# Kernel optimization log

Measured on AMD Instinct MI355X. Metric: run time of the kernel, lower is better.

## Reference

```python
import jax, jax.numpy as jnp
import numpy as np

D, H, DH, L, DFF, V, K = 512, 8, 64, 6, 2048, 256, 5
N = 10240
TAU = 0.1
EPS = 1e-5


def _ln(x, w, b):
    m = x.mean(-1, keepdims=True)
    v = ((x - m) ** 2).mean(-1, keepdims=True)
    return (x - m) * jax.lax.rsqrt(v + EPS) * w + b


def _attn(q_in, kv_in, inw, inb, ow, ob):
    # q_in: [Q, D], kv_in: [M, D]; standard PyTorch MultiheadAttention math
    wq, wk, wv = jnp.split(inw, 3, 0)
    bq, bk, bv = jnp.split(inb, 3)
    q = (q_in @ wq.T + bq).reshape(-1, H, DH)
    k = (kv_in @ wk.T + bk).reshape(-1, H, DH)
    v = (kv_in @ wv.T + bv).reshape(-1, H, DH)
    s = jnp.einsum('qhd,mhd->hqm', q, k) / np.float32(np.sqrt(DH))
    o = jnp.einsum('hqm,mhd->qhd', jax.nn.softmax(s, -1), v).reshape(-1, D)
    return o @ ow.T + ob


def setup_inputs() -> dict:
    key = jax.random.key(0)
    ks = iter(jax.random.split(key, 64))

    def w(shape):
        return jax.random.normal(next(ks), shape, jnp.float32) * 0.02

    inp = {
        'input_bytes': jax.random.randint(next(ks), (N,), 0, V, jnp.int32),
        'emb': w((V, D)),
        'alpha': jnp.float32(0.5),
        'enc_inw': w((L, 3 * D, D)), 'enc_inb': w((L, 3 * D)),
        'enc_ow': w((L, D, D)), 'enc_ob': w((L, D)),
        'enc_w1': w((L, DFF, D)), 'enc_b1': w((L, DFF)),
        'enc_w2': w((L, D, DFF)), 'enc_b2': w((L, D)),
        'enc_ln1w': jnp.ones((L, D)), 'enc_ln1b': jnp.zeros((L, D)),
        'enc_ln2w': jnp.ones((L, D)), 'enc_ln2b': jnp.zeros((L, D)),
        'dec_sa_inw': w((L, 3 * D, D)), 'dec_sa_inb': w((L, 3 * D)),
        'dec_sa_ow': w((L, D, D)), 'dec_sa_ob': w((L, D)),
        'dec_ca_inw': w((L, 3 * D, D)), 'dec_ca_inb': w((L, 3 * D)),
        'dec_ca_ow': w((L, D, D)), 'dec_ca_ob': w((L, D)),
        'dec_w1': w((L, DFF, D)), 'dec_b1': w((L, DFF)),
        'dec_w2': w((L, D, DFF)), 'dec_b2': w((L, D)),
        'dec_ln1w': jnp.ones((L, D)), 'dec_ln1b': jnp.zeros((L, D)),
        'dec_ln2w': jnp.ones((L, D)), 'dec_ln2b': jnp.zeros((L, D)),
        'dec_ln3w': jnp.ones((L, D)), 'dec_ln3b': jnp.zeros((L, D)),
        'out_w': w((V, D)), 'out_b': w((V,)),
    }
    return inp


def reference(input_bytes, emb, alpha, enc_inw, enc_inb, enc_ow, enc_ob,
              enc_w1, enc_b1, enc_w2, enc_b2, enc_ln1w, enc_ln1b, enc_ln2w, enc_ln2b,
              dec_sa_inw, dec_sa_inb, dec_sa_ow, dec_sa_ob,
              dec_ca_inw, dec_ca_inb, dec_ca_ow, dec_ca_ob,
              dec_w1, dec_b1, dec_w2, dec_b2,
              dec_ln1w, dec_ln1b, dec_ln2w, dec_ln2b, dec_ln3w, dec_ln3b,
              out_w, out_b):
    P = input_bytes.shape[0] // K
    patches = input_bytes[:P * K].reshape(P, K)            # fixed k-byte patching
    x = emb[patches].mean(1)                               # mean-pooled patch embeddings [P, D]
    # ---- TransformerEncoder (post-LN, relu FFN, no dropout at eval) ----
    for l in range(L):
        x = _ln(x + _attn(x, x, enc_inw[l], enc_inb[l], enc_ow[l], enc_ob[l]), enc_ln1w[l], enc_ln1b[l])
        ff = jax.nn.relu(x @ enc_w1[l].T + enc_b1[l]) @ enc_w2[l].T + enc_b2[l]
        x = _ln(x + ff, enc_ln2w[l], enc_ln2b[l])
    encoded = x                                            # [P, D]
    # ---- gating + embedding mix (vectorized over the per-patch loop) ----
    gate = jnp.linalg.norm(encoded, axis=-1) > TAU
    tok = emb[patches[:, -1]]
    x = jnp.where(gate[:, None], alpha * encoded + (1.0 - alpha) * tok, tok)  # [P, D]
    # ---- TransformerDecoder: each patch is an independent length-1 target;
    #      self-attn over a single token reduces to out_proj(V(x));
    #      cross-attn attends to the full encoded memory (as in the original loop) ----
    for l in range(L):
        wv = dec_sa_inw[l][2 * D:]
        bv = dec_sa_inb[l][2 * D:]
        sa = (x @ wv.T + bv) @ dec_sa_ow[l].T + dec_sa_ob[l]
        x = _ln(x + sa, dec_ln1w[l], dec_ln1b[l])
        ca = _attn(x, encoded, dec_ca_inw[l], dec_ca_inb[l], dec_ca_ow[l], dec_ca_ob[l])
        x = _ln(x + ca, dec_ln2w[l], dec_ln2b[l])
        ff = jax.nn.relu(x @ dec_w1[l].T + dec_b1[l]) @ dec_w2[l].T + dec_b2[l]
        x = _ln(x + ff, dec_ln3w[l], dec_ln3b[l])
    return x @ out_w.T + out_b                             # [P, V]
```

## Files before the change

### kernel.cpp

```cpp
#include <hip/hip_runtime.h>
#include <hip/hip_bf16.h>
#include <math.h>

#define DD   512
#define HN   8
#define DHD  64
#define LL   6
#define DFF_ 2048
#define VV   256
#define KB_  5
#define PP   2048
#define EPS_ 1e-5f
#define TAU_ 0.1f
#define NS   4
#define KVS  (PP / NS)

typedef __attribute__((ext_vector_type(8))) short bf16x8;
typedef __attribute__((ext_vector_type(4))) short bf16x4;
typedef __attribute__((ext_vector_type(4))) float f32x4;

__device__ __forceinline__ float wave_sum(float v) {
#pragma unroll
  for (int m = 32; m >= 1; m >>= 1) v += __shfl_xor(v, m, 64);
  return v;
}

__device__ __forceinline__ unsigned short f2bf(float f) {
  unsigned u = __float_as_uint(f);
  u += 0x7FFF + ((u >> 16) & 1);
  return (unsigned short)(u >> 16);
}

__device__ __forceinline__ float bf2f(unsigned short u) {
  return __uint_as_float(((unsigned)u) << 16);
}

__device__ __forceinline__ bf16x8 cvt8(float4 a, float4 b) {
  bf16x8 v;
  v[0] = (short)f2bf(a.x); v[1] = (short)f2bf(a.y);
  v[2] = (short)f2bf(a.z); v[3] = (short)f2bf(a.w);
  v[4] = (short)f2bf(b.x); v[5] = (short)f2bf(b.y);
  v[6] = (short)f2bf(b.z); v[7] = (short)f2bf(b.w);
  return v;
}

__device__ __forceinline__ void gload16(const void* g, void* l) {
  __builtin_amdgcn_global_load_lds(
      (const __attribute__((address_space(1))) unsigned int*)g,
      (__attribute__((address_space(3))) unsigned int*)l, 16, 0, 0);
}

#define NSEG 55
struct CvtSeg { const float* src; short* dst; int n; };
struct CvtArgs { CvtSeg seg[NSEG]; };

__global__ __launch_bounds__(256) void convert_bf16_kernel(CvtArgs a) {
  const CvtSeg sg = a.seg[blockIdx.y];
  const int i = ((int)blockIdx.x * 256 + (int)threadIdx.x) * 16;
  if (i >= sg.n) return;
  const float4 x0 = *(const float4*)(sg.src + i);
  const float4 x1 = *(const float4*)(sg.src + i + 4);
  const float4 x2 = *(const float4*)(sg.src + i + 8);
  const float4 x3 = *(const float4*)(sg.src + i + 12);
  *(bf16x8*)(sg.dst + i)     = cvt8(x0, x1);
  *(bf16x8*)(sg.dst + i + 8) = cvt8(x2, x3);
}

__global__ __launch_bounds__(256) void transpose_wv_kernel(const float* __restrict__ sa_inw,
                                                           short* __restrict__ wvt) {
  __shared__ float t[64][65];
  const int l = blockIdx.z;
  const float* S = sa_inw + (size_t)l * 3 * DD * DD + (size_t)2 * DD * DD;
  short* D = wvt + (size_t)l * DD * DD;
  const int bo = blockIdx.y * 64;
  const int bi = blockIdx.x * 64;
  const int r = (int)threadIdx.x >> 2;
  const int c0 = ((int)threadIdx.x & 3) * 16;
#pragma unroll
  for (int j = 0; j < 16; j += 4)
    *(float4*)&t[r][c0 + j] = *(const float4*)&S[(size_t)(bo + r) * DD + bi + c0 + j];
  __syncthreads();
  bf16x8 o0, o1;
#pragma unroll
  for (int j = 0; j < 8; ++j) o0[j] = (short)f2bf(t[c0 + j][r]);
#pragma unroll
  for (int j = 0; j < 8; ++j) o1[j] = (short)f2bf(t[c0 + 8 + j][r]);
  short* dp = &D[(size_t)(bi + r) * DD + bo + c0];
  *(bf16x8*)dp = o0;
  *(bf16x8*)(dp + 8) = o1;
}

__global__ __launch_bounds__(256) void sa_bias_kernel(const float* __restrict__ sa_inb,
                                                      const float* __restrict__ sa_ow,
                                                      const float* __restrict__ sa_ob,
                                                      float* __restrict__ bc) {
  const int gid = (int)blockIdx.x * 4 + ((int)threadIdx.x >> 6);
  const int l = gid >> 9, n = gid & 511;
  const int lane = (int)threadIdx.x & 63;
  const float* wo = sa_ow + (size_t)l * DD * DD + (size_t)n * DD + lane * 8;
  const float* bv = sa_inb + (size_t)l * 3 * DD + 2 * DD + lane * 8;
  float s = 0.f;
#pragma unroll
  for (int j = 0; j < 8; ++j) s += wo[j] * bv[j];
  s = wave_sum(s);
  if (lane == 0) bc[(size_t)l * DD + n] = s + sa_ob[(size_t)l * DD + n];
}

__global__ __launch_bounds__(256) void gemm_wc_kernel(const short* __restrict__ WoBase,
                                                      size_t astr,
                                                      const short* __restrict__ WvT,
                                                      short* __restrict__ Wc) {
  constexpr int BK = 64;
  __shared__ short As[64 * BK];
  __shared__ short Bs[64 * BK];
  const int l = blockIdx.z;
  const short* A = WoBase + (size_t)l * astr;
  const short* W = WvT + (size_t)l * DD * DD;
  short* C = Wc + (size_t)l * DD * DD;
  const int tid = (int)threadIdx.x;
  const int lane = tid & 63;
  const int wid = tid >> 6;
  const int wm = (wid >> 1) * 32;
  const int wn = (wid & 1) * 32;
  const int bm = blockIdx.y * 64;
  const int bn = blockIdx.x * 64;
  const int fr = lane & 15;
  const int kq = lane >> 4;
  const int rs = fr & 7;
  const int srow = lane >> 3;
  const int scg = (lane & 7) ^ srow;

  f32x4 acc[2][2];
#pragma unroll
  for (int i = 0; i < 2; ++i)
#pragma unroll
    for (int j = 0; j < 2; ++j) acc[i][j] = (f32x4){0.f, 0.f, 0.f, 0.f};

  for (int k0 = 0; k0 < DD; k0 += BK) {
    __syncthreads();
#pragma unroll
    for (int is = 0; is < 2; ++is) {
      const int ib = is * 4 + wid;
      gload16(&A[(size_t)(bm + ib * 8 + srow) * DD + k0 + scg * 8], &As[ib * 512]);
      gload16(&W[(size_t)(bn + ib * 8 + srow) * DD + k0 + scg * 8], &Bs[ib * 512]);
    }
    __syncthreads();
#pragma unroll
    for (int s = 0; s < 2; ++s) {
      const int cg = s * 4 + kq;
      const int co = (cg ^ rs) * 8;
      bf16x8 af[2], bf[2];
#pragma unroll
      for (int i = 0; i < 2; ++i) af[i] = *(const bf16x8*)&As[(wm + i * 16 + fr) * BK + co];
#pragma unroll
      for (int j = 0; j < 2; ++j) bf[j] = *(const bf16x8*)&Bs[(wn + j * 16 + fr) * BK + co];
#pragma unroll
      for (int i = 0; i < 2; ++i)
#pragma unroll
        for (int j = 0; j < 2; ++j)
          acc[i][j] = __builtin_amdgcn_mfma_f32_16x16x32_bf16(af[i], bf[j], acc[i][j], 0, 0, 0);
    }
  }
  const int cr = (lane >> 4) * 4;
#pragma unroll
  for (int j = 0; j < 2; ++j) {
    const int col = bn + wn + j * 16 + fr;
#pragma unroll
    for (int i = 0; i < 2; ++i)
#pragma unroll
      for (int r = 0; r < 4; ++r)
        C[(size_t)(bm + wm + i * 16 + cr + r) * DD + col] = (short)f2bf(acc[i][j][r]);
  }
}

__global__ __launch_bounds__(256) void embed_mean_kernel(const int* __restrict__ bytes,
                                                         const float* __restrict__ emb,
                                                         float* __restrict__ x,
                                                         short* __restrict__ xb,
                                                         float* __restrict__ tok) {
  const int p = blockIdx.x;
  const int d = threadIdx.x * 2;
  float a0 = 0.f, a1 = 0.f;
  int last = 0;
#pragma unroll
  for (int k = 0; k < KB_; ++k) {
    const int idx = bytes[p * KB_ + k];
    last = idx;
    const float* e = emb + (size_t)idx * DD + d;
    a0 += e[0]; a1 += e[1];
  }
  a0 *= 0.2f; a1 *= 0.2f;
  x[(size_t)p * DD + d]     = a0;
  x[(size_t)p * DD + d + 1] = a1;
  xb[(size_t)p * DD + d]     = (short)f2bf(a0);
  xb[(size_t)p * DD + d + 1] = (short)f2bf(a1);
  const float* e = emb + (size_t)last * DD + d;
  tok[(size_t)p * DD + d]     = e[0];
  tok[(size_t)p * DD + d + 1] = e[1];
}

template <int BM, int BN, int NSPLIT, int RELU, int WF32, int WBF16, int QS>
__global__ __launch_bounds__(256) void gemm_gl_kernel(
    const short* __restrict__ A, int lda,
    const short* __restrict__ W, int ldw,
    const float* __restrict__ bias,
    float* __restrict__ Cf, short* __restrict__ Cb, int ldc, int Kd,
    size_t pstride) {
  constexpr int BK = 64;
  __shared__ short As[BM * BK];
  __shared__ short Bs[BN * BK];
  constexpr int WM = BM / 2, WN = BN / 2;
  constexpr int MF = WM / 16, NF = WN / 16;
  const int tid = (int)threadIdx.x;
  const int lane = tid & 63;
  const int wid = tid >> 6;
  const int wm = (wid >> 1) * WM;
  const int wn = (wid & 1) * WN;
  const int bm = blockIdx.y * BM;
  const int bn = blockIdx.x * BN;
  const int fr = lane & 15;
  const int kq = lane >> 4;
  const int rs = fr & 7;
  const int srow = lane >> 3;
  const int scg = (lane & 7) ^ srow;

  const int kz = (NSPLIT > 1) ? (int)blockIdx.z : 0;
  const int kbeg = kz * (Kd / NSPLIT);
  const int kend = kbeg + Kd / NSPLIT;

  f32x4 acc[MF][NF];
#pragma unroll
  for (int i = 0; i < MF; ++i)
#pragma unroll
    for (int j = 0; j < NF; ++j) acc[i][j] = (f32x4){0.f, 0.f, 0.f, 0.f};

  for (int k0 = kbeg; k0 < kend; k0 += BK) {
    __syncthreads();
#pragma unroll
    for (int is = 0; is < BM / 32; ++is) {
      const int ib = is * 4 + wid;
      gload16(&A[(size_t)(bm + ib * 8 + srow) * lda + k0 + scg * 8], &As[ib * 512]);
    }
#pragma unroll
    for (int is = 0; is < BN / 32; ++is) {
      const int ib = is * 4 + wid;
      gload16(&W[(size_t)(bn + ib * 8 + srow) * ldw + k0 + scg * 8], &Bs[ib * 512]);
    }
    __syncthreads();
#pragma unroll
    for (int s = 0; s < 2; ++s) {
      const int cg = s * 4 + kq;
      const int co = (cg ^ rs) * 8;
      bf16x8 af[MF], bf[NF];
#pragma unroll
      for (int i = 0; i < MF; ++i)
        af[i] = *(const bf16x8*)&As[(wm + i * 16 + fr) * BK + co];
#pragma unroll
      for (int j = 0; j < NF; ++j)
        bf[j] = *(const bf16x8*)&Bs[(wn + j * 16 + fr) * BK + co];
#pragma unroll
      for (int i = 0; i < MF; ++i)
#pragma unroll
        for (int j = 0; j < NF; ++j)
          acc[i][j] = __builtin_amdgcn_mfma_f32_16x16x32_bf16(af[i], bf[j], acc[i][j], 0, 0, 0);
    }
  }

  const int cr = (lane >> 4) * 4;
  if constexpr (NSPLIT > 1) {
#pragma unroll
    for (int j = 0; j < NF; ++j) {
      const int col = bn + wn + j * 16 + fr;
#pragma unroll
      for (int i = 0; i < MF; ++i)
#pragma unroll
        for (int r = 0; r < 4; ++r) {
          const size_t idx = (size_t)(bm + wm + i * 16 + cr + r) * ldc + col;
          if (WF32) Cf[(size_t)kz * pstride + idx] = acc[i][j][r];
          else      Cb[(size_t)kz * pstride + idx] = (short)f2bf(acc[i][j][r]);
        }
    }
  } else {
#pragma unroll
    for (int j = 0; j < NF; ++j) {
      const int col = bn + wn + j * 16 + fr;
      const float bb = bias[col];
      const float sc = (QS && col < DD) ? 0.125f : 1.f;
#pragma unroll
      for (int i = 0; i < MF; ++i) {
#pragma unroll
        for (int r = 0; r < 4; ++r) {
          float v = (acc[i][j][r] + bb) * sc;
          if (RELU) v = fmaxf(v, 0.f);
          const size_t idx = (size_t)(bm + wm + i * 16 + cr + r) * ldc + col;
          if (WF32) Cf[idx] = v;
          if (WBF16) Cb[idx] = (short)f2bf(v);
        }
      }
    }
  }
}

__global__ __launch_bounds__(256) void gemm_ca_kernel(
    const short* __restrict__ Aq, const short* __restrict__ Akv,
    const short* __restrict__ Wfull, const float* __restrict__ bias,
    short* __restrict__ Cb) {
  constexpr int BK = 64;
  __shared__ short As[64 * BK];
  __shared__ short Bs[64 * BK];
  const int bx = (int)blockIdx.x;
  const int part_kv = bx >= 8;
  const short* A = part_kv ? Akv : Aq;
  const int wrow0 = part_kv ? DD + (bx - 8) * 64 : bx * 64;
  const float sc = part_kv ? 1.f : 0.125f;
  const int tid = (int)threadIdx.x;
  const int lane = tid & 63;
  const int wid = tid >> 6;
  const int wm = (wid >> 1) * 32;
  const int wn = (wid & 1) * 32;
  const int bm = blockIdx.y * 64;
  const int fr = lane & 15;
  const int kq = lane >> 4;
  const int rs = fr & 7;
  const int srow = lane >> 3;
  const int scg = (lane & 7) ^ srow;

  f32x4 acc[2][2];
#pragma unroll
  for (int i = 0; i < 2; ++i)
#pragma unroll
    for (int j = 0; j < 2; ++j) acc[i][j] = (f32x4){0.f, 0.f, 0.f, 0.f};

  for (int k0 = 0; k0 < DD; k0 += BK) {
    __syncthreads();
#pragma unroll
    for (int is = 0; is < 2; ++is) {
      const int ib = is * 4 + wid;
      gload16(&A[(size_t)(bm + ib * 8 + srow) * DD + k0 + scg * 8], &As[ib * 512]);
      gload16(&Wfull[(size_t)(wrow0 + ib * 8 + srow) * DD + k0 + scg * 8], &Bs[ib * 512]);
    }
    __syncthreads();
#pragma unroll
    for (int s = 0; s < 2; ++s) {
      const int cg = s * 4 + kq;
      const int co = (cg ^ rs) * 8;
      bf16x8 af[2], bf[2];
#pragma unroll
      for (int i = 0; i < 2; ++i) af[i] = *(const bf16x8*)&As[(wm + i * 16 + fr) * BK + co];
#pragma unroll
      for (int j = 0; j < 2; ++j) bf[j] = *(const bf16x8*)&Bs[(wn + j * 16 + fr) * BK + co];
#pragma unroll
      for (int i = 0; i < 2; ++i)
#pragma unroll
        for (int j = 0; j < 2; ++j)
          acc[i][j] = __builtin_amdgcn_mfma_f32_16x16x32_bf16(af[i], bf[j], acc[i][j], 0, 0, 0);
    }
  }
  const int cr = (lane >> 4) * 4;
#pragma unroll
  for (int j = 0; j < 2; ++j) {
    const int col = wrow0 + wn + j * 16 + fr;
    const float bb = bias[col];
#pragma unroll
    for (int i = 0; i < 2; ++i)
#pragma unroll
      for (int r = 0; r < 4; ++r)
        Cb[(size_t)(bm + wm + i * 16 + cr + r) * (3 * DD) + col] =
            (short)f2bf((acc[i][j][r] + bb) * sc);
  }
}

__global__ __launch_bounds__(256) void flash_attn_mfma_kernel(const short* __restrict__ qkvb,
                                                              short* __restrict__ Opart,
                                                              float* __restrict__ stats) {
  constexpr int LS = 72;
  __shared__ short Ks[64 * LS];
  __shared__ short Vt[64 * LS];
  __shared__ short Ps[64 * LS];
  const int h = blockIdx.y;
  const int q0 = blockIdx.x * 64;
  const int sp = blockIdx.z;
  const int tid = (int)threadIdx.x;
  const int lane = tid & 63;
  const int wid = tid >> 6;
  const int fr = lane & 15;
  const int g = lane >> 4;
  const int kg = g * 8;

  bf16x8 qf[2];
  {
    const short* src = qkvb + (size_t)(q0 + wid * 16 + fr) * (3 * DD) + h * DHD + kg;
    qf[0] = *(const bf16x8*)src;
    qf[1] = *(const bf16x8*)(src + 32);
  }

  f32x4 acc_o[4];
#pragma unroll
  for (int df = 0; df < 4; ++df) acc_o[df] = (f32x4){0.f, 0.f, 0.f, 0.f};
  float mreg = -INFINITY, lsum = 0.f;

  const int sr8 = tid >> 3;
  const int sc8 = (tid & 7) * 8;
  const int vk2 = (tid & 31) * 2;
  const int vd8 = (tid >> 5) * 8;

  for (int t = 0; t < KVS / 64; ++t) {
    const int k0 = sp * KVS + t * 64;
    __syncthreads();
    {
#pragma unroll
      for (int p = 0; p < 64; p += 32)
        *(bf16x8*)&Ks[(sr8 + p) * LS + sc8] =
            *(const bf16x8*)&qkvb[(size_t)(k0 + sr8 + p) * (3 * DD) + DD + h * DHD + sc8];
      const short* vbase = qkvb + (size_t)(k0 + vk2) * (3 * DD) + 2 * DD + h * DHD + vd8;
      const bf16x8 v0 = *(const bf16x8*)vbase;
      const bf16x8 v1 = *(const bf16x8*)(vbase + 3 * DD);
#pragma unroll
      for (int j = 0; j < 8; ++j) {
        const unsigned pk = ((unsigned)(unsigned short)v0[j]) |
                            (((unsigned)(unsigned short)v1[j]) << 16);
        *(unsigned*)&Vt[(vd8 + j) * LS + vk2] = pk;
      }
    }
    __syncthreads();

    f32x4 st[4];
#pragma unroll
    for (int nf = 0; nf < 4; ++nf) st[nf] = (f32x4){0.f, 0.f, 0.f, 0.f};
    __builtin_amdgcn_s_setprio(1);
#pragma unroll
    for (int nf = 0; nf < 4; ++nf) {
      const bf16x8 kf0 = *(const bf16x8*)&Ks[(nf * 16 + fr) * LS + kg];
      const bf16x8 kf1 = *(const bf16x8*)&Ks[(nf * 16 + fr) * LS + kg + 32];
      st[nf] = __builtin_amdgcn_mfma_f32_16x16x32_bf16(kf0, qf[0], st[nf], 0, 0, 0);
      st[nf] = __builtin_amdgcn_mfma_f32_16x16x32_bf16(kf1, qf[1], st[nf], 0, 0, 0);
    }
    __builtin_amdgcn_s_setprio(0);

    float mx = st[0][0];
#pragma unroll
    for (int nf = 0; nf < 4; ++nf)
#pragma unroll
      for (int i = 0; i < 4; ++i) mx = fmaxf(mx, st[nf][i]);
    mx = fmaxf(mx, __shfl_xor(mx, 16, 64));
    mx = fmaxf(mx, __shfl_xor(mx, 32, 64));
    const float mn = fmaxf(mreg, mx);
    const float corr = __expf(mreg - mn);
    mreg = mn;
    float pv[4][4];
    float sum = 0.f;
#pragma unroll
    for (int nf = 0; nf < 4; ++nf)
#pragma unroll
      for (int i = 0; i < 4; ++i) {
        pv[nf][i] = __expf(st[nf][i] - mn);
        sum += pv[nf][i];
      }
    sum += __shfl_xor(sum, 16, 64);
    sum += __shfl_xor(sum, 32, 64);
    lsum = lsum * corr + sum;

    float corr_acc[4];
#pragma unroll
    for (int i = 0; i < 4; ++i)
      corr_acc[i] = __shfl(corr, (lane & 48) | (g * 4 + i), 64);
#pragma unroll
    for (int df = 0; df < 4; ++df) {
      acc_o[df][0] *= corr_acc[0]; acc_o[df][1] *= corr_acc[1];
      acc_o[df][2] *= corr_acc[2]; acc_o[df][3] *= corr_acc[3];
    }

#pragma unroll
    for (int nf = 0; nf < 4; ++nf) {
      bf16x4 pw;
#pragma unroll
      for (int i = 0; i < 4; ++i) pw[i] = (short)f2bf(pv[nf][i]);
      *(bf16x4*)&Ps[(wid * 16 + fr) * LS + nf * 16 + g * 4] = pw;
    }
    asm volatile("s_waitcnt lgkmcnt(0)" ::: "memory");

    const bf16x8 pa0 = *(const bf16x8*)&Ps[(wid * 16 + fr) * LS + kg];
    const bf16x8 pa1 = *(const bf16x8*)&Ps[(wid * 16 + fr) * LS + kg + 32];
    __builtin_amdgcn_s_setprio(1);
#pragma unroll
    for (int df = 0; df < 4; ++df) {
      const bf16x8 vb0 = *(const bf16x8*)&Vt[(df * 16 + fr) * LS + kg];
      const bf16x8 vb1 = *(const bf16x8*)&Vt[(df * 16 + fr) * LS + kg + 32];
      acc_o[df] = __builtin_amdgcn_mfma_f32_16x16x32_bf16(pa0, vb0, acc_o[df], 0, 0, 0);
      acc_o[df] = __builtin_amdgcn_mfma_f32_16x16x32_bf16(pa1, vb1, acc_o[df], 0, 0, 0);
    }
    __builtin_amdgcn_s_setprio(0);
  }

  const int orow = q0 + wid * 16 + g * 4;
#pragma unroll
  for (int df = 0; df < 4; ++df)
#pragma unroll
    for (int i = 0; i < 4; ++i)
      Opart[((size_t)sp * PP + orow + i) * DD + h * DHD + df * 16 + fr] =
          (short)f2bf(acc_o[df][i]);
  if (g == 0) {
    const size_t si = (((size_t)sp * PP + q0 + wid * 16 + fr) * HN + h) * 2;
    stats[si]     = mreg;
    stats[si + 1] = lsum;
  }
}

__global__ __launch_bounds__(256) void attn_combine_kernel(const short* __restrict__ Opart,
                                                           const float* __restrict__ stats,
                                                           short* __restrict__ outb) {
  const int row = blockIdx.x * 4 + ((int)threadIdx.x >> 6);
  const int lane = (int)threadIdx.x & 63;
  const int d0 = lane * 8;
  const int h = d0 >> 6;
  float m[NS], l[NS];
  float M = -INFINITY;
#pragma unroll
  for (int s = 0; s < NS; ++s) {
    const size_t si = (((size_t)s * PP + row) * HN + h) * 2;
    m[s] = stats[si]; l[s] = stats[si + 1];
    M = fmaxf(M, m[s]);
  }
  float L = 0.f;
  float o[8];
#pragma unroll
  for (int j = 0; j < 8; ++j) o[j] = 0.f;
#pragma unroll
  for (int s = 0; s < NS; ++s) {
    const float e = __expf(m[s] - M);
    L += l[s] * e;
    const bf16x8 v = *(const bf16x8*)&Opart[((size_t)s * PP + row) * DD + d0];
#pragma unroll
    for (int j = 0; j < 8; ++j) o[j] += bf2f((unsigned short)v[j]) * e;
  }
  const float inv = 1.f / L;
  bf16x8 ob;
#pragma unroll
  for (int j = 0; j < 8; ++j) ob[j] = (short)f2bf(o[j] * inv);
  *(bf16x8*)&outb[(size_t)row * DD + d0] = ob;
}

__global__ __launch_bounds__(256) void ln_residual_kernel(const float* __restrict__ xin,
                                                          const short* __restrict__ pA,
                                                          const short* __restrict__ pB,
                                                          const float* __restrict__ gb,
                                                          const float* __restrict__ w,
                                                          const float* __restrict__ b,
                                                          float* __restrict__ out,
                                                          short* __restrict__ outb) {
  const int row = blockIdx.x * 4 + (threadIdx.x >> 6);
  const int lane = threadIdx.x & 63;
  const size_t base = (size_t)row * DD + lane * 8;
  float v[8];
  {
    const float4 a0 = *(const float4*)&xin[base];
    const float4 a1 = *(const float4*)&xin[base + 4];
    const bf16x8 r = *(const bf16x8*)&pA[base];
    const bf16x8 s = *(const bf16x8*)&pB[base];
    const float4 g0 = *(const float4*)&gb[lane * 8];
    const float4 g1 = *(const float4*)&gb[lane * 8 + 4];
    v[0] = a0.x + bf2f((unsigned short)r[0]) + bf2f((unsigned short)s[0]) + g0.x;
    v[1] = a0.y + bf2f((unsigned short)r[1]) + bf2f((unsigned short)s[1]) + g0.y;
    v[2] = a0.z + bf2f((unsigned short)r[2]) + bf2f((unsigned short)s[2]) + g0.z;
    v[3] = a0.w + bf2f((unsigned short)r[3]) + bf2f((unsigned short)s[3]) + g0.w;
    v[4] = a1.x + bf2f((unsigned short)r[4]) + bf2f((unsigned short)s[4]) + g1.x;
    v[5] = a1.y + bf2f((unsigned short)r[5]) + bf2f((unsigned short)s[5]) + g1.y;
    v[6] = a1.z + bf2f((unsigned short)r[6]) + bf2f((unsigned short)s[6]) + g1.z;
    v[7] = a1.w + bf2f((unsigned short)r[7]) + bf2f((unsigned short)s[7]) + g1.w;
  }
  float sum = 0.f;
#pragma unroll
  for (int j = 0; j < 8; ++j) sum += v[j];
  sum = wave_sum(sum);
  const float mean = sum * (1.f / DD);
  float sq = 0.f;
#pragma unroll
  for (int j = 0; j < 8; ++j) { const float dd = v[j] - mean; sq += dd * dd; }
  sq = wave_sum(sq);
  const float rstd = rsqrtf(sq * (1.f / DD) + EPS_);
  const float* wp = w + lane * 8;
  const float* bp = b + lane * 8;
  float o[8];
#pragma unroll
  for (int j = 0; j < 8; ++j) o[j] = (v[j] - mean) * rstd * wp[j] + bp[j];
  *(float4*)&out[base] = *(float4*)&o[0];
  *(float4*)&out[base + 4] = *(float4*)&o[4];
  bf16x8 ob;
#pragma unroll
  for (int j = 0; j < 8; ++j) ob[j] = (short)f2bf(o[j]);
  *(bf16x8*)&outb[base] = ob;
}

__global__ __launch_bounds__(256) void ln_gate_kernel(const float* __restrict__ xin,
                                                      const short* __restrict__ pA,
                                                      const short* __restrict__ pB,
                                                      const float* __restrict__ gb,
                                                      const float* __restrict__ w,
                                                      const float* __restrict__ b,
                                                      const float* __restrict__ tok,
                                                      const float* __restrict__ alpha_p,
                                                      float* __restrict__ xout,
                                                      short* __restrict__ xb,
                                                      short* __restrict__ encb) {
  const int row = blockIdx.x * 4 + (threadIdx.x >> 6);
  const int lane = threadIdx.x & 63;
  const size_t base = (size_t)row * DD + lane * 8;
  float v[8];
  {
    const float4 a0 = *(const float4*)&xin[base];
    const float4 a1 = *(const float4*)&xin[base + 4];
    const bf16x8 r = *(const bf16x8*)&pA[base];
    const bf16x8 s = *(const bf16x8*)&pB[base];
    const float4 g0 = *(const float4*)&gb[lane * 8];
    const float4 g1 = *(const float4*)&gb[lane * 8 + 4];
    v[0] = a0.x + bf2f((unsigned short)r[0]) + bf2f((unsigned short)s[0]) + g0.x;
    v[1] = a0.y + bf2f((unsigned short)r[1]) + bf2f((unsigned short)s[1]) + g0.y;
    v[2] = a0.z + bf2f((unsigned short)r[2]) + bf2f((unsigned short)s[2]) + g0.z;
    v[3] = a0.w + bf2f((unsigned short)r[3]) + bf2f((unsigned short)s[3]) + g0.w;
    v[4] = a1.x + bf2f((unsigned short)r[4]) + bf2f((unsigned short)s[4]) + g1.x;
    v[5] = a1.y + bf2f((unsigned short)r[5]) + bf2f((unsigned short)s[5]) + g1.y;
    v[6] = a1.z + bf2f((unsigned short)r[6]) + bf2f((unsigned short)s[6]) + g1.z;
    v[7] = a1.w + bf2f((unsigned short)r[7]) + bf2f((unsigned short)s[7]) + g1.w;
  }
  float sum = 0.f;
#pragma unroll
  for (int j = 0; j < 8; ++j) sum += v[j];
  sum = wave_sum(sum);
  const float mean = sum * (1.f / DD);
  float sq = 0.f;
#pragma unroll
  for (int j = 0; j < 8; ++j) { const float dd = v[j] - mean; sq += dd * dd; }
  sq = wave_sum(sq);
  const float rstd = rsqrtf(sq * (1.f / DD) + EPS_);
  const float* wp = w + lane * 8;
  const float* bp = b + lane * 8;
  float e[8];
#pragma unroll
  for (int j = 0; j < 8; ++j) e[j] = (v[j] - mean) * rstd * wp[j] + bp[j];
  bf16x8 eb;
#pragma unroll
  for (int j = 0; j < 8; ++j) eb[j] = (short)f2bf(e[j]);
  *(bf16x8*)&encb[base] = eb;
  float nsq = 0.f;
#pragma unroll
  for (int j = 0; j < 8; ++j) nsq += e[j] * e[j];
  nsq = wave_sum(nsq);
  const bool gate = nsq > TAU_ * TAU_;
  const float a = *alpha_p;
  float t[8];
  {
    const float4 b0 = *(const float4*)&tok[base];
    const float4 b1 = *(const float4*)&tok[base + 4];
    t[0] = b0.x; t[1] = b0.y; t[2] = b0.z; t[3] = b0.w;
    t[4] = b1.x; t[5] = b1.y; t[6] = b1.z; t[7] = b1.w;
  }
  float o[8];
#pragma unroll
  for (int j = 0; j < 8; ++j) o[j] = gate ? (a * e[j] + (1.f - a) * t[j]) : t[j];
  *(float4*)&xout[base] = *(float4*)&o[0];
  *(float4*)&xout[base + 4] = *(float4*)&o[4];
  bf16x8 ob;
#pragma unroll
  for (int j = 0; j < 8; ++j) ob[j] = (short)f2bf(o[j]);
  *(bf16x8*)&xb[base] = ob;
}

__global__ __launch_bounds__(256) void out_combine_kernel(const float* __restrict__ P0,
                                                          const float* __restrict__ P1,
                                                          const float* __restrict__ bias,
                                                          float* __restrict__ out) {
  const size_t i = ((size_t)blockIdx.x * 256 + threadIdx.x) * 4;
  const int col = (int)(i % VV);
  const float4 a = *(const float4*)&P0[i];
  const float4 b = *(const float4*)&P1[i];
  const float4 c = *(const float4*)&bias[col];
  float4 o;
  o.x = a.x + b.x + c.x; o.y = a.y + b.y + c.y;
  o.z = a.z + b.z + c.z; o.w = a.w + b.w + c.w;
  *(float4*)&out[i] = o;
}

extern "C" void kernel_launch(void* const* d_in, const int* in_sizes, int n_in,
                              void* d_out, int out_size, void* d_ws, size_t ws_size,
                              hipStream_t stream) {
  const int*   bytes    = (const int*)d_in[0];
  const float* emb      = (const float*)d_in[1];
  const float* alpha    = (const float*)d_in[2];
  const float* enc_inw  = (const float*)d_in[3];
  const float* enc_inb  = (const float*)d_in[4];
  const float* enc_ow   = (const float*)d_in[5];
  const float* enc_ob   = (const float*)d_in[6];
  const float* enc_w1   = (const float*)d_in[7];
  const float* enc_b1   = (const float*)d_in[8];
  const float* enc_w2   = (const float*)d_in[9];
  const float* enc_b2   = (const float*)d_in[10];
  const float* enc_ln1w = (const float*)d_in[11];
  const float* enc_ln1b = (const float*)d_in[12];
  const float* enc_ln2w = (const float*)d_in[13];
  const float* enc_ln2b = (const float*)d_in[14];
  const float* dec_sa_inw = (const float*)d_in[15];
  const float* dec_sa_inb = (const float*)d_in[16];
  const float* dec_sa_ow  = (const float*)d_in[17];
  const float* dec_sa_ob  = (const float*)d_in[18];
  const float* dec_ca_inw = (const float*)d_in[19];
  const float* dec_ca_inb = (const float*)d_in[20];
  const float* dec_ca_ow  = (const float*)d_in[21];
  const float* dec_ca_ob  = (const float*)d_in[22];
  const float* dec_w1   = (const float*)d_in[23];
  const float* dec_b1   = (const float*)d_in[24];
  const float* dec_w2   = (const float*)d_in[25];
  const float* dec_b2   = (const float*)d_in[26];
  const float* dec_ln1w = (const float*)d_in[27];
  const float* dec_ln1b = (const float*)d_in[28];
  const float* dec_ln2w = (const float*)d_in[29];
  const float* dec_ln2b = (const float*)d_in[30];
  const float* dec_ln3w = (const float*)d_in[31];
  const float* dec_ln3b = (const float*)d_in[32];
  const float* out_w    = (const float*)d_in[33];
  const float* out_b    = (const float*)d_in[34];

  float* fp = (float*)d_ws;
  float* x     = fp;  fp += (size_t)PP * DD;
  float* tok   = fp;  fp += (size_t)PP * DD;
  float* stats = fp;  fp += (size_t)NS * PP * HN * 2;
  float* outP  = fp;  fp += (size_t)2 * PP * VV;
  float* bcbuf = fp;  fp += (size_t)LL * DD;
  short* sp = (short*)fp;
  short* OpartB  = sp;  sp += (size_t)NS * PP * DD;
  short* tmpB    = sp;  sp += (size_t)2 * PP * DD;
  short* x_bf    = sp;  sp += (size_t)PP * DD;
  short* enc_bf  = sp;  sp += (size_t)PP * DD;
  short* qkv_bf  = sp;  sp += (size_t)PP * 3 * DD;
  short* attno_bf= sp;  sp += (size_t)PP * DD;
  short* ffh_bf  = sp;  sp += (size_t)PP * DFF_;
  short* wvT     = sp;  sp += (size_t)LL * DD * DD;
  short* wcM     = sp;  sp += (size_t)LL * DD * DD;
  short* warena  = sp;

  CvtArgs ca;
  size_t eoff[LL][4], doff[LL][5], ooff;
  size_t dec_start = 0, dec_stride = 0;
  {
    int si = 0;
    size_t off = 0;
    const size_t n0 = 3 * DD * DD, n1 = DD * DD, n2 = (size_t)DFF_ * DD, n3 = (size_t)DD * DFF_;
    for (int l = 0; l < LL; ++l) {
      ca.seg[si++] = {enc_inw + (size_t)l * n0, warena + off, (int)n0}; eoff[l][0] = off; off += n0;
      ca.seg[si++] = {enc_ow  + (size_t)l * n1, warena + off, (int)n1}; eoff[l][1] = off; off += n1;
      ca.seg[si++] = {enc_w1  + (size_t)l * n2, warena + off, (int)n2}; eoff[l][2] = off; off += n2;
      ca.seg[si++] = {enc_w2  + (size_t)l * n3, warena + off, (int)n3}; eoff[l][3] = off; off += n3;
    }
    dec_start = off;
    for (int l = 0; l < LL; ++l) {
      const size_t o0 = off;
      ca.seg[si++] = {dec_sa_ow  + (size_t)l * n1, warena + off, (int)n1}; doff[l][0] = off; off += n1;
      ca.seg[si++] = {dec_ca_inw + (size_t)l * n0, warena + off, (int)n0}; doff[l][1] = off; off += n0;
      ca.seg[si++] = {dec_ca_ow  + (size_t)l * n1, warena + off, (int)n1}; doff[l][2] = off; off += n1;
      ca.seg[si++] = {dec_w1     + (size_t)l * n2, warena + off, (int)n2}; doff[l][3] = off; off += n2;
      ca.seg[si++] = {dec_w2     + (size_t)l * n3, warena + off, (int)n3}; doff[l][4] = off; off += n3;
      if (l == 0) dec_stride = off - o0; (void)o0;
    }
    ca.seg[si++] = {out_w, warena + off, VV * DD}; ooff = off;
  }

  const dim3 b256(256);
  const dim3 gFA(PP / 64, HN, NS);
  const dim3 gQKV(3 * DD / 64, PP / 128);
  const dim3 gFF1(DFF_ / 64, PP / 128);
  const dim3 gS(DD / 64, PP / 64, 2);
  const dim3 gCA(24, PP / 64);
  const dim3 gOUTg(VV / 64, PP / 64, 2);
  const size_t psD = (size_t)PP * DD;
  const size_t psV = (size_t)PP * VV;

  convert_bf16_kernel<<<dim3(256, NSEG), b256, 0, stream>>>(ca);
  transpose_wv_kernel<<<dim3(8, 8, LL), b256, 0, stream>>>(dec_sa_inw, wvT);
  sa_bias_kernel<<<(LL * DD) / 4, b256, 0, stream>>>(dec_sa_inb, dec_sa_ow, dec_sa_ob, bcbuf);
  gemm_wc_kernel<<<dim3(8, 8, LL), b256, 0, stream>>>(warena + dec_start, dec_stride, wvT, wcM);
  embed_mean_kernel<<<PP, b256, 0, stream>>>(bytes, emb, x, x_bf, tok);

  for (int l = 0; l < LL; ++l) {
    const float* inb = enc_inb + (size_t)l * 3 * DD;
    const float* ob  = enc_ob  + (size_t)l * DD;
    const float* b1  = enc_b1  + (size_t)l * DFF_;
    const float* b2  = enc_b2  + (size_t)l * DD;

    gemm_gl_kernel<128, 64, 1, 0, 0, 1, 1><<<gQKV, b256, 0, stream>>>(
        x_bf, DD, warena + eoff[l][0], DD, inb, nullptr, qkv_bf, 3 * DD, DD, 0);
    flash_attn_mfma_kernel<<<gFA, b256, 0, stream>>>(qkv_bf, OpartB, stats);
    attn_combine_kernel<<<PP / 4, b256, 0, stream>>>(OpartB, stats, attno_bf);
    gemm_gl_kernel<64, 64, 2, 0, 0, 0, 0><<<gS, b256, 0, stream>>>(
        attno_bf, DD, warena + eoff[l][1], DD, nullptr, nullptr, tmpB, DD, DD, psD);
    ln_residual_kernel<<<PP / 4, b256, 0, stream>>>(
        x, tmpB, tmpB + psD, ob, enc_ln1w + (size_t)l * DD, enc_ln1b + (size_t)l * DD, x, x_bf);
    gemm_gl_kernel<128, 64, 1, 1, 0, 1, 0><<<gFF1, b256, 0, stream>>>(
        x_bf, DD, warena + eoff[l][2], DD, b1, nullptr, ffh_bf, DFF_, DD, 0);
    gemm_gl_kernel<64, 64, 2, 0, 0, 0, 0><<<gS, b256, 0, stream>>>(
        ffh_bf, DFF_, warena + eoff[l][3], DFF_, nullptr, nullptr, tmpB, DD, DFF_, psD);
    if (l + 1 < LL) {
      ln_residual_kernel<<<PP / 4, b256, 0, stream>>>(
          x, tmpB, tmpB + psD, b2, enc_ln2w + (size_t)l * DD, enc_ln2b + (size_t)l * DD, x, x_bf);
    } else {
      ln_gate_kernel<<<PP / 4, b256, 0, stream>>>(
          x, tmpB, tmpB + psD, b2, enc_ln2w + (size_t)l * DD, enc_ln2b + (size_t)l * DD,
          tok, alpha, x, x_bf, enc_bf);
    }
  }

  for (int l = 0; l < LL; ++l) {
    const float* ca_inb = dec_ca_inb + (size_t)l * 3 * DD;
    const float* ca_ob  = dec_ca_ob + (size_t)l * DD;
    const float* b1 = dec_b1 + (size_t)l * DFF_;
    const float* b2 = dec_b2 + (size_t)l * DD;

    gemm_gl_kernel<64, 64, 2, 0, 0, 0, 0><<<gS, b256, 0, stream>>>(
        x_bf, DD, wcM + (size_t)l * DD * DD, DD, nullptr, nullptr, tmpB, DD, DD, psD);
    ln_residual_kernel<<<PP / 4, b256, 0, stream>>>(
        x, tmpB, tmpB + psD, bcbuf + (size_t)l * DD,
        dec_ln1w + (size_t)l * DD, dec_ln1b + (size_t)l * DD, x, x_bf);

    gemm_ca_kernel<<<gCA, b256, 0, stream>>>(
        x_bf, enc_bf, warena + doff[l][1], ca_inb, qkv_bf);
    flash_attn_mfma_kernel<<<gFA, b256, 0, stream>>>(qkv_bf, OpartB, stats);
    attn_combine_kernel<<<PP / 4, b256, 0, stream>>>(OpartB, stats, attno_bf);
    gemm_gl_kernel<64, 64, 2, 0, 0, 0, 0><<<gS, b256, 0, stream>>>(
        attno_bf, DD, warena + doff[l][2], DD, nullptr, nullptr, tmpB, DD, DD, psD);
    ln_residual_kernel<<<PP / 4, b256, 0, stream>>>(
        x, tmpB, tmpB + psD, ca_ob, dec_ln2w + (size_t)l * DD, dec_ln2b + (size_t)l * DD, x, x_bf);

    gemm_gl_kernel<128, 64, 1, 1, 0, 1, 0><<<gFF1, b256, 0, stream>>>(
        x_bf, DD, warena + doff[l][3], DD, b1, nullptr, ffh_bf, DFF_, DD, 0);
    gemm_gl_kernel<64, 64, 2, 0, 0, 0, 0><<<gS, b256, 0, stream>>>(
        ffh_bf, DFF_, warena + doff[l][4], DFF_, nullptr, nullptr, tmpB, DD, DFF_, psD);
    ln_residual_kernel<<<PP / 4, b256, 0, stream>>>(
        x, tmpB, tmpB + psD, b2, dec_ln3w + (size_t)l * DD, dec_ln3b + (size_t)l * DD, x, x_bf);
  }

  gemm_gl_kernel<64, 64, 2, 0, 1, 0, 0><<<gOUTg, b256, 0, stream>>>(
      x_bf, DD, warena + ooff, DD, nullptr, outP, nullptr, VV, DD, psV);
  out_combine_kernel<<<(PP * VV / 4) / 256, b256, 0, stream>>>(
      outP, outP + psV, out_b, (float*)d_out);
}
```

Measured before the change: 1.041 ms.

## Double GEMM K-tile to 128 and load attention K tiles via direct-to-LDS swizzled loads

The bf16 MFMA GEMM now stages a K-slice of 128 instead of 64 per iteration, with a new 16-way XOR swizzle for the wider rows. This halves the number of barrier and load rounds per output tile. In the flash-attention kernel, K tiles are now loaded with gload16 (global-to-LDS) into an unpadded, XOR-swizzled buffer instead of going through registers into a padded one. The cost is double the GEMM shared memory, which may reduce occupancy, and the new swizzle may cause bank conflicts.

Result: faster. 989.8 us (-4.9%).

```diff
diff --git a/kernel.cpp b/kernel.cpp
--- a/kernel.cpp
+++ b/kernel.cpp
@@ -206,7 +206,7 @@
     const float* __restrict__ bias,
     float* __restrict__ Cf, short* __restrict__ Cb, int ldc, int Kd,
     size_t pstride) {
-  constexpr int BK = 64;
+  constexpr int BK = 128;
   __shared__ short As[BM * BK];
   __shared__ short Bs[BN * BK];
   constexpr int WM = BM / 2, WN = BN / 2;
@@ -220,9 +220,8 @@
   const int bn = blockIdx.x * BN;
   const int fr = lane & 15;
   const int kq = lane >> 4;
-  const int rs = fr & 7;
-  const int srow = lane >> 3;
-  const int scg = (lane & 7) ^ srow;
+  const int srow = lane >> 4;
+  const int sc16 = lane & 15;
 
   const int kz = (NSPLIT > 1) ? (int)blockIdx.z : 0;
   const int kbeg = kz * (Kd / NSPLIT);
@@ -237,20 +236,23 @@
   for (int k0 = kbeg; k0 < kend; k0 += BK) {
     __syncthreads();
 #pragma unroll
-    for (int is = 0; is < BM / 32; ++is) {
+    for (int is = 0; is < BM / 16; ++is) {
       const int ib = is * 4 + wid;
-      gload16(&A[(size_t)(bm + ib * 8 + srow) * lda + k0 + scg * 8], &As[ib * 512]);
-    }
-#pragma unroll
-    for (int is = 0; is < BN / 32; ++is) {
+      const int row = ib * 4 + srow;
+      const int cg = sc16 ^ (row & 15);
+      gload16(&A[(size_t)(bm + row) * lda + k0 + cg * 8], &As[ib * 512]);
+    }
+#pragma unroll
+    for (int is = 0; is < BN / 16; ++is) {
       const int ib = is * 4 + wid;
-      gload16(&W[(size_t)(bn + ib * 8 + srow) * ldw + k0 + scg * 8], &Bs[ib * 512]);
+      const int row = ib * 4 + srow;
+      const int cg = sc16 ^ (row & 15);
+      gload16(&W[(size_t)(bn + row) * ldw + k0 + cg * 8], &Bs[ib * 512]);
     }
     __syncthreads();
 #pragma unroll
-    for (int s = 0; s < 2; ++s) {
-      const int cg = s * 4 + kq;
-      const int co = (cg ^ rs) * 8;
+    for (int s = 0; s < 4; ++s) {
+      const int co = ((s * 4 + kq) ^ fr) * 8;
       bf16x8 af[MF], bf[NF];
 #pragma unroll
       for (int i = 0; i < MF; ++i)
@@ -374,7 +376,7 @@
                                                               short* __restrict__ Opart,
                                                               float* __restrict__ stats) {
   constexpr int LS = 72;
-  __shared__ short Ks[64 * LS];
+  __shared__ short Ks[64 * 64];
   __shared__ short Vt[64 * LS];
   __shared__ short Ps[64 * LS];
   const int h = blockIdx.y;
@@ -386,6 +388,7 @@
   const int fr = lane & 15;
   const int g = lane >> 4;
   const int kg = g * 8;
+  const int rs3 = fr & 7;
 
   bf16x8 qf[2];
   {
@@ -399,8 +402,8 @@
   for (int df = 0; df < 4; ++df) acc_o[df] = (f32x4){0.f, 0.f, 0.f, 0.f};
   float mreg = -INFINITY, lsum = 0.f;
 
-  const int sr8 = tid >> 3;
-  const int sc8 = (tid & 7) * 8;
+  const int srow8 = lane >> 3;
+  const int sscg = (lane & 7) ^ srow8;
   const int vk2 = (tid & 31) * 2;
   const int vd8 = (tid >> 5) * 8;
 
@@ -409,9 +412,11 @@
     __syncthreads();
     {
 #pragma unroll
-      for (int p = 0; p < 64; p += 32)
-        *(bf16x8*)&Ks[(sr8 + p) * LS + sc8] =
-            *(const bf16x8*)&qkvb[(size_t)(k0 + sr8 + p) * (3 * DD) + DD + h * DHD + sc8];
+      for (int p = 0; p < 2; ++p) {
+        const int rb = p * 32 + wid * 8;
+        gload16(&qkvb[(size_t)(k0 + rb + srow8) * (3 * DD) + DD + h * DHD + sscg * 8],
+                &Ks[rb * 64]);
+      }
       const short* vbase = qkvb + (size_t)(k0 + vk2) * (3 * DD) + 2 * DD + h * DHD + vd8;
       const bf16x8 v0 = *(const bf16x8*)vbase;
       const bf16x8 v1 = *(const bf16x8*)(vbase + 3 * DD);
@@ -430,8 +435,9 @@
     __builtin_amdgcn_s_setprio(1);
 #pragma unroll
     for (int nf = 0; nf < 4; ++nf) {
-      const bf16x8 kf0 = *(const bf16x8*)&Ks[(nf * 16 + fr) * LS + kg];
-      const bf16x8 kf1 = *(const bf16x8*)&Ks[(nf * 16 + fr) * LS + kg + 32];
+      const int krow = (nf * 16 + fr) * 64;
+      const bf16x8 kf0 = *(const bf16x8*)&Ks[krow + ((g ^ rs3) * 8)];
+      const bf16x8 kf1 = *(const bf16x8*)&Ks[krow + (((g + 4) ^ rs3) * 8)];
       st[nf] = __builtin_amdgcn_mfma_f32_16x16x32_bf16(kf0, qf[0], st[nf], 0, 0, 0);
       st[nf] = __builtin_amdgcn_mfma_f32_16x16x32_bf16(kf1, qf[1], st[nf], 0, 0, 0);
     }
```
